# Kernel optimization log

Hardware: AMD Instinct MI355X
Metric: run time of the kernel (lower is better)

The kernel has to match this reference:

```python
import jax, jax.numpy as jnp
import numpy as np

N_GRP = 2048   # n groups
L = 64         # kv slots per group
Q = 4096       # total queries (nq.sum())
D = 256        # d_q = d_k = d_h
DZ = 256       # attention projection dim d_z
DX = 256       # token embedding dim
NTYP = 64      # relation types
NTOK = 50000   # token vocab
M = 131072     # memory tokens
G = 16384      # scatter_sum groups
B = 1024       # examples for scatter_min


def setup_inputs() -> dict:
    key = jax.random.key(0)
    ks = jax.random.split(key, 16)
    q = jax.random.normal(ks[0], (Q, D), jnp.float32)
    k = jax.random.normal(ks[1], (N_GRP, L, D), jnp.float32)
    m = jax.random.bernoulli(ks[2], 0.7, (N_GRP, L))
    m = m.at[:, 0].set(True)  # guarantee >=1 valid slot per group
    # per-query group index == repeat_interleave(arange(n), nq) with nq = 2
    qgrp = jnp.repeat(jnp.arange(N_GRP, dtype=jnp.int32), Q // N_GRP)
    mem = jax.random.randint(ks[3], (M,), 0, NTOK, jnp.int32)
    grp = jnp.sort(jax.random.randint(ks[4], (M,), 0, G, jnp.int32))
    pos2grp = jax.random.randint(ks[5], (N_GRP, L), 0, G, jnp.int32)
    typ = jax.random.randint(ks[6], (Q, NTYP), 0, 2, jnp.int32).astype(bool)
    idx = jnp.sort(jax.random.randint(ks[7], (Q,), 0, B, jnp.int32))
    s = lambda d: 1.0 / np.sqrt(d).astype(np.float32)
    emb = jax.random.normal(ks[8], (NTOK, DX), jnp.float32)
    Wq = jax.random.normal(ks[9], (DZ, D), jnp.float32) * s(D)
    bq = jnp.zeros((DZ,), jnp.float32)
    Wk = jax.random.normal(ks[10], (DZ, D), jnp.float32) * s(D)
    bk = jnp.zeros((DZ,), jnp.float32)
    Wrel = jax.random.normal(ks[11], (NTYP, D + DX), jnp.float32) * s(D + DX)
    brel = jnp.zeros((NTYP,), jnp.float32)
    return dict(q=q, k=k, emb=emb, Wq=Wq, bq=bq, Wk=Wk, bk=bk, Wrel=Wrel,
                brel=brel, m=m, qgrp=qgrp, mem=mem, grp=grp, pos2grp=pos2grp,
                typ=typ, idx=idx)


def reference(q, k, emb, Wq, bq, Wk, bk, Wrel, brel, m, qgrp, mem, grp,
              pos2grp, typ, idx):
    # x_all = scatter_sum(tok_embedding(mem), grp, 0)[pos2grp] : (n, l, dx)
    x_all = jax.ops.segment_sum(emb[mem], grp, num_segments=G)[pos2grp]
    # Attention (ragged masked softmax over l, per-query group gather)
    qz = q @ Wq.T + bq                      # (Q, dz)
    kz = k @ Wk.T + bk                      # (n, l, dz)
    s = jnp.einsum('qd,qld->ql', qz, kz[qgrp]) / np.sqrt(DZ).astype(np.float32)
    s = jnp.where(m[qgrp], s, -jnp.inf)     # masked_fill(~m, -inf)
    p = jax.nn.softmax(s, axis=1)           # softmax over l
    att = jnp.einsum('ql,qld->qd', p, x_all[qgrp])   # (Q, dx)
    logit = jnp.concatenate([q, att], axis=-1) @ Wrel.T + brel  # (Q, n_typ)
    gt = logit > 0
    eq = gt == typ
    acc = eq.astype(jnp.float32).mean()
    em = jax.ops.segment_min(eq.all(1).astype(jnp.int32), idx, num_segments=B)
    emr = em.astype(jnp.float32).mean()
    # binary_cross_entropy_with_logits, reduction='sum', / len(m)
    nll = (jnp.logaddexp(0.0, logit) - logit * typ.astype(logit.dtype)).sum() / N_GRP
    return (logit, acc, emr, nll, em)
```

## Files before the change

### kernel.cpp

```cpp
#include <hip/hip_runtime.h>
#include <hip/hip_bf16.h>
#include <math.h>

#define N_GRP 2048
#define LSLOT 64
#define NQ    4096
#define DIM   256
#define NTYPE 64
#define MMEM  131072
#define GSEG  16384
#define BEX   1024

#define OFF_SEG   0u
#define OFF_QW    4194304u
#define OFF_MT    5242880u
#define OFF_VB    5308416u
#define OFF_WB    5308672u
#define OFF_SB    5308928u
#define OFF_EM    5308936u
#define OFF_CNT   5309960u
#define OFF_NLL   5309964u
#define OFF_FLAG  5309966u

#define OUT_ACC 262144
#define OUT_EMR 262145
#define OUT_NLL 262146
#define OUT_EM  262147

__device__ __forceinline__ bool rd_bool(const void* p, int i, int mode) {
  if (mode == 0) return ((const int*)p)[i] != 0;
  if (mode == 1) return ((const unsigned char*)p)[i] != 0;
  return ((const float*)p)[i] != 0.f;
}

__global__ __launch_bounds__(256)
void k_pre(const float* __restrict__ Wq, const float* __restrict__ bq,
           const float* __restrict__ Wk, const float* __restrict__ bk,
           const void* __restrict__ typ, float* __restrict__ ws) {
  int b = blockIdx.x, t = threadIdx.x;
  if (b < 256) {
    int j = b;
    float acc = 0.f;
    #pragma unroll 8
    for (int z = 0; z < 256; ++z)
      acc += Wk[z * 256 + t] * Wq[z * 256 + j];
    ws[OFF_MT + (unsigned)j * 256 + t] = acc;
  } else if (b == 256) {
    float a = 0.f;
    #pragma unroll 8
    for (int z = 0; z < 256; ++z) a += Wq[z * 256 + t] * bk[z];
    ws[OFF_VB + t] = a;
  } else if (b == 257) {
    float a = 0.f;
    #pragma unroll 8
    for (int z = 0; z < 256; ++z) a += Wk[z * 256 + t] * bq[z];
    ws[OFF_WB + t] = a;
    __shared__ float red[256];
    red[t] = bq[t] * bk[t];
    __syncthreads();
    for (int st = 128; st; st >>= 1) { if (t < st) red[t] += red[t + st]; __syncthreads(); }
    if (t == 0) ws[OFF_SB] = red[0];
  } else {
    __shared__ int fl_f, fl_b;
    if (t == 0) { fl_f = 0; fl_b = 0; }
    __syncthreads();
    for (int i = t; i < 4096; i += 256) {
      unsigned wv = ((const unsigned*)typ)[i];
      if (wv == 0x3F800000u) atomicOr(&fl_f, 1);
      else if (wv > 1u)      atomicOr(&fl_b, 1);
    }
    __syncthreads();
    int* em = (int*)(ws + OFF_EM);
    for (int i = t; i < BEX; i += 256) em[i] = 0x7FFFFFFF;
    if (t == 0) {
      *(int*)(ws + OFF_FLAG) = fl_f ? 2 : (fl_b ? 1 : 0);
      *(int*)(ws + OFF_CNT) = 0;
      *(double*)(ws + OFF_NLL) = 0.0;
    }
  }
}

__global__ __launch_bounds__(256)
void k_segqw(const float* __restrict__ emb, const int* __restrict__ mem,
             const int* __restrict__ grp, const float* __restrict__ q,
             float* __restrict__ ws) {
  int t = threadIdx.x;
  if (blockIdx.x < GSEG / 4) {
    int lane = t & 63, w = t >> 6;
    int g = blockIdx.x * 4 + w;
    int lo = 0, hi = MMEM;
    while (lo < hi) { int mid = (lo + hi) >> 1; if (grp[mid] < g) lo = mid + 1; else hi = mid; }
    int lo2 = lo, hi2 = MMEM;
    while (lo2 < hi2) { int mid = (lo2 + hi2) >> 1; if (grp[mid] < g + 1) lo2 = mid + 1; else hi2 = mid; }
    int n = lo2 - lo;
    int nv = n < 64 ? n : 64;
    int tok = (lane < nv) ? mem[lo + lane] : 0;
    float4 acc = {0.f, 0.f, 0.f, 0.f};
    int r = 0;
    for (; r + 4 <= nv; r += 4) {
      int t0 = __shfl(tok, r + 0), t1 = __shfl(tok, r + 1);
      int t2 = __shfl(tok, r + 2), t3 = __shfl(tok, r + 3);
      float4 v0 = *(const float4*)(emb + (size_t)t0 * 256 + lane * 4);
      float4 v1 = *(const float4*)(emb + (size_t)t1 * 256 + lane * 4);
      float4 v2 = *(const float4*)(emb + (size_t)t2 * 256 + lane * 4);
      float4 v3 = *(const float4*)(emb + (size_t)t3 * 256 + lane * 4);
      acc.x += (v0.x + v1.x) + (v2.x + v3.x);
      acc.y += (v0.y + v1.y) + (v2.y + v3.y);
      acc.z += (v0.z + v1.z) + (v2.z + v3.z);
      acc.w += (v0.w + v1.w) + (v2.w + v3.w);
    }
    for (; r < nv; ++r) {
      int tr = __shfl(tok, r);
      float4 v = *(const float4*)(emb + (size_t)tr * 256 + lane * 4);
      acc.x += v.x; acc.y += v.y; acc.z += v.z; acc.w += v.w;
    }
    for (int rr = lo + 64; rr < lo2; ++rr) {
      int tr = mem[rr];
      float4 v = *(const float4*)(emb + (size_t)tr * 256 + lane * 4);
      acc.x += v.x; acc.y += v.y; acc.z += v.z; acc.w += v.w;
    }
    *(float4*)(ws + OFF_SEG + (size_t)g * 256 + lane * 4) = acc;
  } else {
    int b = blockIdx.x - GSEG / 4;
    int r0 = b * 8;
    const float* MT = ws + OFF_MT;
    float acc[8];
    float wbv = ws[OFF_WB + t];
    #pragma unroll
    for (int r = 0; r < 8; ++r) acc[r] = wbv;
    for (int j = 0; j < 256; j += 4) {
      float m0 = MT[(j + 0) * 256 + t];
      float m1 = MT[(j + 1) * 256 + t];
      float m2 = MT[(j + 2) * 256 + t];
      float m3 = MT[(j + 3) * 256 + t];
      #pragma unroll
      for (int r = 0; r < 8; ++r) {
        float4 q4 = *(const float4*)(q + (size_t)(r0 + r) * 256 + j);
        acc[r] += q4.x * m0 + q4.y * m1 + q4.z * m2 + q4.w * m3;
      }
    }
    #pragma unroll
    for (int r = 0; r < 8; ++r) ws[OFF_QW + (unsigned)(r0 + r) * 256 + t] = acc[r];
  }
}

__global__ __launch_bounds__(256)
void k_attn(const float* __restrict__ q, const float* __restrict__ k,
            const float* __restrict__ Wrel, const float* __restrict__ brel,
            const void* __restrict__ mmask, const int* __restrict__ pos2grp,
            const void* __restrict__ typ, const int* __restrict__ idx,
            float* __restrict__ ws, float* __restrict__ out) {
  int g = blockIdx.x;
  int t = threadIdx.x;
  int lane = t & 63, w = t >> 6;
  __shared__ float qw_l[2][256], qr_l[2][256], att_l[2][256];
  __shared__ float s_raw[2][64], p_l[2][64];
  __shared__ float att_p[4][2][64][4];
  __shared__ float cq_l[2];
  __shared__ float nll_l;
  __shared__ int eqcnt_l, all_l[2];
  const int q0 = 2 * g;
  const int mode = *(const int*)(ws + OFF_FLAG);

  qw_l[0][t] = ws[OFF_QW + (unsigned)q0 * 256 + t];
  qw_l[1][t] = ws[OFF_QW + (unsigned)(q0 + 1) * 256 + t];
  qr_l[0][t] = q[(size_t)q0 * 256 + t];
  qr_l[1][t] = q[(size_t)(q0 + 1) * 256 + t];
  if (t == 0) { eqcnt_l = 0; nll_l = 0.f; }
  if (w < 2) {
    const float* qrow = q + (size_t)(q0 + w) * 256;
    float p = 0.f;
    #pragma unroll
    for (int u = 0; u < 4; ++u) p += qrow[lane + 64 * u] * ws[OFF_VB + lane + 64 * u];
    for (int off = 32; off; off >>= 1) p += __shfl_xor(p, off);
    if (lane == 0) cq_l[w] = p + ws[OFF_SB];
  }
  __syncthreads();

  {
    int sl = w * 16 + (lane >> 2);
    int c4 = lane & 3;
    const float* kr = k + (size_t)g * LSLOT * 256 + (size_t)sl * 256 + c4 * 4;
    float s0 = 0.f, s1 = 0.f;
    #pragma unroll
    for (int j = 0; j < 16; ++j) {
      float4 kv = *(const float4*)(kr + j * 16);
      float4 w0 = *(const float4*)&qw_l[0][j * 16 + c4 * 4];
      float4 w1 = *(const float4*)&qw_l[1][j * 16 + c4 * 4];
      s0 += kv.x * w0.x + kv.y * w0.y + kv.z * w0.z + kv.w * w0.w;
      s1 += kv.x * w1.x + kv.y * w1.y + kv.z * w1.z + kv.w * w1.w;
    }
    s0 += __shfl_xor(s0, 1); s0 += __shfl_xor(s0, 2);
    s1 += __shfl_xor(s1, 1); s1 += __shfl_xor(s1, 2);
    if (c4 == 0) { s_raw[0][sl] = s0; s_raw[1][sl] = s1; }
  }
  __syncthreads();

  if (w < 2) {
    bool valid = rd_bool(mmask, g * LSLOT + lane, mode);
    float v = valid ? (s_raw[w][lane] + cq_l[w]) * 0.0625f : -INFINITY;
    float mx = v;
    for (int off = 32; off; off >>= 1) mx = fmaxf(mx, __shfl_xor(mx, off));
    float e = expf(v - mx);
    float ssum = e;
    for (int off = 32; off; off >>= 1) ssum += __shfl_xor(ssum, off);
    p_l[w][lane] = e / ssum;
  }
  __syncthreads();

  {
    float4 a0 = {0.f,0.f,0.f,0.f}, a1 = {0.f,0.f,0.f,0.f};
    const float* seg = ws + OFF_SEG;
    const int* pg = pos2grp + g * LSLOT;
    #pragma unroll 4
    for (int li = 0; li < 16; ++li) {
      int l = li * 4 + w;
      float p0 = p_l[0][l], p1 = p_l[1][l];
      if (p0 == 0.f && p1 == 0.f) continue;
      int row = pg[l];
      float4 v = *(const float4*)(seg + (size_t)row * 256 + lane * 4);
      a0.x += p0 * v.x; a0.y += p0 * v.y; a0.z += p0 * v.z; a0.w += p0 * v.w;
      a1.x += p1 * v.x; a1.y += p1 * v.y; a1.z += p1 * v.z; a1.w += p1 * v.w;
    }
    *(float4*)&att_p[w][0][lane][0] = a0;
    *(float4*)&att_p[w][1][lane][0] = a1;
  }
  __syncthreads();
  {
    int dl = t >> 2, dc = t & 3;
    #pragma unroll
    for (int qi = 0; qi < 2; ++qi)
      att_l[qi][t] = att_p[0][qi][dl][dc] + att_p[1][qi][dl][dc]
                   + att_p[2][qi][dl][dc] + att_p[3][qi][dl][dc];
  }
  __syncthreads();

  {
    int qi = w >> 1;
    int c4 = lane & 3;
    #pragma unroll
    for (int h = 0; h < 2; ++h) {
      int tt = (w & 1) * 32 + h * 16 + (lane >> 2);
      const float* wr = Wrel + (size_t)tt * 512 + c4 * 4;
      float s = 0.f;
      #pragma unroll
      for (int j = 0; j < 16; ++j) {
        float4 wv = *(const float4*)(wr + j * 16);
        float4 xv = *(const float4*)&qr_l[qi][j * 16 + c4 * 4];
        s += wv.x * xv.x + wv.y * xv.y + wv.z * xv.z + wv.w * xv.w;
      }
      #pragma unroll
      for (int j = 0; j < 16; ++j) {
        float4 wv = *(const float4*)(wr + 1024 + j * 16);
        float4 xv = *(const float4*)&att_l[qi][j * 16 + c4 * 4];
        s += wv.x * xv.x + wv.y * xv.y + wv.z * xv.z + wv.w * xv.w;
      }
      s += __shfl_xor(s, 1); s += __shfl_xor(s, 2);
      if (c4 == 0) s_raw[qi][tt] = s;
    }
  }
  __syncthreads();

  if (w < 2) {
    int qi = w;
    float lg = s_raw[qi][lane] + brel[lane];
    out[(size_t)(q0 + qi) * NTYPE + lane] = lg;
    bool gt = lg > 0.f;
    bool tv = rd_bool(typ, (q0 + qi) * NTYPE + lane, mode);
    bool eqv = (gt == tv);
    unsigned long long mask = __ballot(eqv);
    float nllp = fmaxf(lg, 0.f) + log1pf(expf(-fabsf(lg))) - (tv ? lg : 0.f);
    for (int off = 32; off; off >>= 1) nllp += __shfl_xor(nllp, off);
    if (lane == 0) {
      all_l[qi] = (mask == 0xFFFFFFFFFFFFFFFFull) ? 1 : 0;
      atomicAdd(&eqcnt_l, (int)__popcll(mask));
      atomicAdd(&nll_l, nllp);
    }
  }
  __syncthreads();
  if (t == 0) {
    atomicAdd((int*)(ws + OFF_CNT), eqcnt_l);
    atomicAdd((double*)(ws + OFF_NLL), (double)nll_l);
    int* em = (int*)(ws + OFF_EM);
    atomicMin(&em[idx[q0]], all_l[0]);
    atomicMin(&em[idx[q0 + 1]], all_l[1]);
  }
}

__global__ __launch_bounds__(256)
void k_fin(float* __restrict__ ws, float* __restrict__ out) {
  __shared__ float red[256];
  int t = threadIdx.x;
  const int* em = (const int*)(ws + OFF_EM);
  float s = 0.f;
  for (int i = t; i < BEX; i += 256) {
    float v = (float)em[i];
    out[OUT_EM + i] = v;
    s += v;
  }
  red[t] = s; __syncthreads();
  for (int st = 128; st; st >>= 1) { if (t < st) red[t] += red[t + st]; __syncthreads(); }
  if (t == 0) {
    out[OUT_ACC] = (float)(*(const int*)(ws + OFF_CNT)) / (float)(NQ * NTYPE);
    out[OUT_EMR] = red[0] / (float)BEX;
    out[OUT_NLL] = (float)((*(const double*)(ws + OFF_NLL)) / (double)N_GRP);
  }
}

extern "C" void kernel_launch(void* const* d_in, const int* in_sizes, int n_in,
                              void* d_out, int out_size, void* d_ws, size_t ws_size,
                              hipStream_t stream) {
  const float* q    = (const float*)d_in[0];
  const float* k    = (const float*)d_in[1];
  const float* emb  = (const float*)d_in[2];
  const float* Wq   = (const float*)d_in[3];
  const float* bq   = (const float*)d_in[4];
  const float* Wk   = (const float*)d_in[5];
  const float* bk   = (const float*)d_in[6];
  const float* Wrel = (const float*)d_in[7];
  const float* brel = (const float*)d_in[8];
  const void* mmask   = d_in[9];
  const int* mem      = (const int*)d_in[11];
  const int* grp      = (const int*)d_in[12];
  const int* pos2grp  = (const int*)d_in[13];
  const void* typ     = d_in[14];
  const int* idx      = (const int*)d_in[15];
  float* ws  = (float*)d_ws;
  float* out = (float*)d_out;

  k_pre  <<<259,            256, 0, stream>>>(Wq, bq, Wk, bk, typ, ws);
  k_segqw<<<GSEG/4 + NQ/8,  256, 0, stream>>>(emb, mem, grp, q, ws);
  k_attn <<<N_GRP,          256, 0, stream>>>(q, k, Wrel, brel, mmask, pos2grp, typ, idx, ws, out);
  k_fin  <<<1,              256, 0, stream>>>(ws, out);
}
```

Measured before the change: 386.8 us.

## Split attention kernel, precompute segment pointers, skip masked key slots

Replaces the per-group binary searches with a CSR pointer array built in the prep kernel, used when the workspace is large enough. Moves the query-bias dot product into the projection kernel. Splits the fused attention kernel into a scoring kernel, which skips loading key rows for masked slots, and a separate attention-plus-logit kernel. The softmax probabilities are passed between the two through the output buffer. This cuts search and key-load traffic, but adds a kernel launch and a global round trip.

```diff
diff --git a/kernel.cpp b/kernel.cpp
--- a/kernel.cpp
+++ b/kernel.cpp
@@ -21,6 +21,9 @@
 #define OFF_CNT   5309960u
 #define OFF_NLL   5309964u
 #define OFF_FLAG  5309966u
+#define OFF_CQ    5310208u
+#define OFF_PTR   5314304u
+#define WS_NEED_PTR ((size_t)(OFF_PTR + GSEG + 1) * 4)
 
 #define OUT_ACC 262144
 #define OUT_EMR 262145
@@ -36,15 +39,19 @@
 __global__ __launch_bounds__(256)
 void k_pre(const float* __restrict__ Wq, const float* __restrict__ bq,
            const float* __restrict__ Wk, const float* __restrict__ bk,
-           const void* __restrict__ typ, float* __restrict__ ws) {
+           const void* __restrict__ typ, const int* __restrict__ grp,
+           float* __restrict__ ws, int use_ptr) {
   int b = blockIdx.x, t = threadIdx.x;
   if (b < 256) {
     int j = b;
-    float acc = 0.f;
-    #pragma unroll 8
-    for (int z = 0; z < 256; ++z)
-      acc += Wk[z * 256 + t] * Wq[z * 256 + j];
-    ws[OFF_MT + (unsigned)j * 256 + t] = acc;
+    float a0 = 0.f, a1 = 0.f, a2 = 0.f, a3 = 0.f;
+    for (int z = 0; z < 256; z += 4) {
+      a0 += Wk[(z + 0) * 256 + t] * Wq[(z + 0) * 256 + j];
+      a1 += Wk[(z + 1) * 256 + t] * Wq[(z + 1) * 256 + j];
+      a2 += Wk[(z + 2) * 256 + t] * Wq[(z + 2) * 256 + j];
+      a3 += Wk[(z + 3) * 256 + t] * Wq[(z + 3) * 256 + j];
+    }
+    ws[OFF_MT + (unsigned)j * 256 + t] = (a0 + a1) + (a2 + a3);
   } else if (b == 256) {
     float a = 0.f;
     #pragma unroll 8
@@ -60,7 +67,7 @@
     __syncthreads();
     for (int st = 128; st; st >>= 1) { if (t < st) red[t] += red[t + st]; __syncthreads(); }
     if (t == 0) ws[OFF_SB] = red[0];
-  } else {
+  } else if (b == 258) {
     __shared__ int fl_f, fl_b;
     if (t == 0) { fl_f = 0; fl_b = 0; }
     __syncthreads();
@@ -77,21 +84,37 @@
       *(int*)(ws + OFF_CNT) = 0;
       *(double*)(ws + OFF_NLL) = 0.0;
     }
+  } else {
+    if (!use_ptr) return;
+    int i = (b - 259) * 256 + t;
+    int gi = grp[i];
+    int gp = (i == 0) ? -1 : grp[i - 1];
+    int* ptr = (int*)(ws + OFF_PTR);
+    for (int gg = gp + 1; gg <= gi; ++gg) ptr[gg] = i;
+    if (i == MMEM - 1)
+      for (int gg = gi + 1; gg <= GSEG; ++gg) ptr[gg] = MMEM;
   }
 }
 
 __global__ __launch_bounds__(256)
 void k_segqw(const float* __restrict__ emb, const int* __restrict__ mem,
              const int* __restrict__ grp, const float* __restrict__ q,
-             float* __restrict__ ws) {
+             float* __restrict__ ws, int use_ptr) {
   int t = threadIdx.x;
   if (blockIdx.x < GSEG / 4) {
     int lane = t & 63, w = t >> 6;
     int g = blockIdx.x * 4 + w;
-    int lo = 0, hi = MMEM;
-    while (lo < hi) { int mid = (lo + hi) >> 1; if (grp[mid] < g) lo = mid + 1; else hi = mid; }
-    int lo2 = lo, hi2 = MMEM;
-    while (lo2 < hi2) { int mid = (lo2 + hi2) >> 1; if (grp[mid] < g + 1) lo2 = mid + 1; else hi2 = mid; }
+    int lo, lo2;
+    if (use_ptr) {
+      const int* ptr = (const int*)(ws + OFF_PTR);
+      lo = ptr[g]; lo2 = ptr[g + 1];
+    } else {
+      int l0 = 0, h0 = MMEM;
+      while (l0 < h0) { int mid = (l0 + h0) >> 1; if (grp[mid] < g) l0 = mid + 1; else h0 = mid; }
+      lo = l0; int l1 = l0, h1 = MMEM;
+      while (l1 < h1) { int mid = (l1 + h1) >> 1; if (grp[mid] < g + 1) l1 = mid + 1; else h1 = mid; }
+      lo2 = l1;
+    }
     int n = lo2 - lo;
     int nv = n < 64 ? n : 64;
     int tok = (lane < nv) ? mem[lo + lane] : 0;
@@ -124,88 +147,101 @@
     int b = blockIdx.x - GSEG / 4;
     int r0 = b * 8;
     const float* MT = ws + OFF_MT;
-    float acc[8];
+    float acc[8], cq[8];
     float wbv = ws[OFF_WB + t];
     #pragma unroll
-    for (int r = 0; r < 8; ++r) acc[r] = wbv;
+    for (int r = 0; r < 8; ++r) { acc[r] = wbv; cq[r] = 0.f; }
     for (int j = 0; j < 256; j += 4) {
       float m0 = MT[(j + 0) * 256 + t];
       float m1 = MT[(j + 1) * 256 + t];
       float m2 = MT[(j + 2) * 256 + t];
       float m3 = MT[(j + 3) * 256 + t];
+      float4 vb4 = *(const float4*)(ws + OFF_VB + j);
       #pragma unroll
       for (int r = 0; r < 8; ++r) {
         float4 q4 = *(const float4*)(q + (size_t)(r0 + r) * 256 + j);
         acc[r] += q4.x * m0 + q4.y * m1 + q4.z * m2 + q4.w * m3;
+        cq[r] += q4.x * vb4.x + q4.y * vb4.y + q4.z * vb4.z + q4.w * vb4.w;
       }
     }
     #pragma unroll
     for (int r = 0; r < 8; ++r) ws[OFF_QW + (unsigned)(r0 + r) * 256 + t] = acc[r];
-  }
-}
-
-__global__ __launch_bounds__(256)
-void k_attn(const float* __restrict__ q, const float* __restrict__ k,
-            const float* __restrict__ Wrel, const float* __restrict__ brel,
-            const void* __restrict__ mmask, const int* __restrict__ pos2grp,
-            const void* __restrict__ typ, const int* __restrict__ idx,
-            float* __restrict__ ws, float* __restrict__ out) {
-  int g = blockIdx.x;
-  int t = threadIdx.x;
+    if (t == 0) {
+      float sb = ws[OFF_SB];
+      #pragma unroll
+      for (int r = 0; r < 8; ++r) ws[OFF_CQ + r0 + r] = cq[r] + sb;
+    }
+  }
+}
+
+__global__ __launch_bounds__(256)
+void k_score(const float* __restrict__ k, const void* __restrict__ mmask,
+             float* __restrict__ ws, float* __restrict__ out) {
+  int g = blockIdx.x, t = threadIdx.x;
   int lane = t & 63, w = t >> 6;
-  __shared__ float qw_l[2][256], qr_l[2][256], att_l[2][256];
-  __shared__ float s_raw[2][64], p_l[2][64];
-  __shared__ float att_p[4][2][64][4];
-  __shared__ float cq_l[2];
-  __shared__ float nll_l;
-  __shared__ int eqcnt_l, all_l[2];
+  __shared__ float qw_l[2][256];
+  __shared__ float s_raw[2][64];
   const int q0 = 2 * g;
   const int mode = *(const int*)(ws + OFF_FLAG);
 
   qw_l[0][t] = ws[OFF_QW + (unsigned)q0 * 256 + t];
   qw_l[1][t] = ws[OFF_QW + (unsigned)(q0 + 1) * 256 + t];
-  qr_l[0][t] = q[(size_t)q0 * 256 + t];
-  qr_l[1][t] = q[(size_t)(q0 + 1) * 256 + t];
-  if (t == 0) { eqcnt_l = 0; nll_l = 0.f; }
-  if (w < 2) {
-    const float* qrow = q + (size_t)(q0 + w) * 256;
-    float p = 0.f;
-    #pragma unroll
-    for (int u = 0; u < 4; ++u) p += qrow[lane + 64 * u] * ws[OFF_VB + lane + 64 * u];
-    for (int off = 32; off; off >>= 1) p += __shfl_xor(p, off);
-    if (lane == 0) cq_l[w] = p + ws[OFF_SB];
-  }
   __syncthreads();
 
   {
     int sl = w * 16 + (lane >> 2);
     int c4 = lane & 3;
-    const float* kr = k + (size_t)g * LSLOT * 256 + (size_t)sl * 256 + c4 * 4;
-    float s0 = 0.f, s1 = 0.f;
-    #pragma unroll
-    for (int j = 0; j < 16; ++j) {
-      float4 kv = *(const float4*)(kr + j * 16);
-      float4 w0 = *(const float4*)&qw_l[0][j * 16 + c4 * 4];
-      float4 w1 = *(const float4*)&qw_l[1][j * 16 + c4 * 4];
-      s0 += kv.x * w0.x + kv.y * w0.y + kv.z * w0.z + kv.w * w0.w;
-      s1 += kv.x * w1.x + kv.y * w1.y + kv.z * w1.z + kv.w * w1.w;
-    }
-    s0 += __shfl_xor(s0, 1); s0 += __shfl_xor(s0, 2);
-    s1 += __shfl_xor(s1, 1); s1 += __shfl_xor(s1, 2);
-    if (c4 == 0) { s_raw[0][sl] = s0; s_raw[1][sl] = s1; }
+    bool valid = rd_bool(mmask, g * LSLOT + sl, mode);
+    if (valid) {
+      const float* kr = k + (size_t)g * LSLOT * 256 + (size_t)sl * 256 + c4 * 4;
+      float s0 = 0.f, s1 = 0.f;
+      #pragma unroll
+      for (int j = 0; j < 16; ++j) {
+        float4 kv = *(const float4*)(kr + j * 16);
+        float4 w0 = *(const float4*)&qw_l[0][j * 16 + c4 * 4];
+        float4 w1 = *(const float4*)&qw_l[1][j * 16 + c4 * 4];
+        s0 += kv.x * w0.x + kv.y * w0.y + kv.z * w0.z + kv.w * w0.w;
+        s1 += kv.x * w1.x + kv.y * w1.y + kv.z * w1.z + kv.w * w1.w;
+      }
+      s0 += __shfl_xor(s0, 1); s0 += __shfl_xor(s0, 2);
+      s1 += __shfl_xor(s1, 1); s1 += __shfl_xor(s1, 2);
+      if (c4 == 0) { s_raw[0][sl] = s0; s_raw[1][sl] = s1; }
+    }
   }
   __syncthreads();
 
   if (w < 2) {
     bool valid = rd_bool(mmask, g * LSLOT + lane, mode);
-    float v = valid ? (s_raw[w][lane] + cq_l[w]) * 0.0625f : -INFINITY;
+    float cq = ws[OFF_CQ + q0 + w];
+    float v = valid ? (s_raw[w][lane] + cq) * 0.0625f : -INFINITY;
     float mx = v;
     for (int off = 32; off; off >>= 1) mx = fmaxf(mx, __shfl_xor(mx, off));
     float e = expf(v - mx);
     float ssum = e;
     for (int off = 32; off; off >>= 1) ssum += __shfl_xor(ssum, off);
-    p_l[w][lane] = e / ssum;
-  }
+    out[(size_t)(q0 + w) * NTYPE + lane] = e / ssum;
+  }
+}
+
+__global__ __launch_bounds__(256)
+void k_attlogit(const float* __restrict__ q, const float* __restrict__ Wrel,
+                const float* __restrict__ brel, const int* __restrict__ pos2grp,
+                const void* __restrict__ typ, const int* __restrict__ idx,
+                float* __restrict__ ws, float* __restrict__ out) {
+  int g = blockIdx.x, t = threadIdx.x;
+  int lane = t & 63, w = t >> 6;
+  __shared__ float qr_l[2][256], att_l[2][256];
+  __shared__ float p_l[2][64], lg_l[2][64];
+  __shared__ float att_p[4][2][64][4];
+  __shared__ float nll_l;
+  __shared__ int eqcnt_l, all_l[2];
+  const int q0 = 2 * g;
+  const int mode = *(const int*)(ws + OFF_FLAG);
+
+  qr_l[0][t] = q[(size_t)q0 * 256 + t];
+  qr_l[1][t] = q[(size_t)(q0 + 1) * 256 + t];
+  if (w < 2) p_l[w][lane] = out[(size_t)(q0 + w) * NTYPE + lane];
+  if (t == 0) { eqcnt_l = 0; nll_l = 0.f; }
   __syncthreads();
 
   {
@@ -256,14 +292,14 @@
         s += wv.x * xv.x + wv.y * xv.y + wv.z * xv.z + wv.w * xv.w;
       }
       s += __shfl_xor(s, 1); s += __shfl_xor(s, 2);
-      if (c4 == 0) s_raw[qi][tt] = s;
+      if (c4 == 0) lg_l[qi][tt] = s;
     }
   }
   __syncthreads();
 
   if (w < 2) {
     int qi = w;
-    float lg = s_raw[qi][lane] + brel[lane];
+    float lg = lg_l[qi][lane] + brel[lane];
     out[(size_t)(q0 + qi) * NTYPE + lane] = lg;
     bool gt = lg > 0.f;
     bool tv = rd_bool(typ, (q0 + qi) * NTYPE + lane, mode);
@@ -327,9 +363,11 @@
   const int* idx      = (const int*)d_in[15];
   float* ws  = (float*)d_ws;
   float* out = (float*)d_out;
-
-  k_pre  <<<259,            256, 0, stream>>>(Wq, bq, Wk, bk, typ, ws);
-  k_segqw<<<GSEG/4 + NQ/8,  256, 0, stream>>>(emb, mem, grp, q, ws);
-  k_attn <<<N_GRP,          256, 0, stream>>>(q, k, Wrel, brel, mmask, pos2grp, typ, idx, ws, out);
-  k_fin  <<<1,              256, 0, stream>>>(ws, out);
-}
+  int use_ptr = (ws_size >= WS_NEED_PTR) ? 1 : 0;
+
+  k_pre     <<<259 + MMEM/256, 256, 0, stream>>>(Wq, bq, Wk, bk, typ, grp, ws, use_ptr);
+  k_segqw   <<<GSEG/4 + NQ/8,  256, 0, stream>>>(emb, mem, grp, q, ws, use_ptr);
+  k_score   <<<N_GRP,          256, 0, stream>>>(k, mmask, ws, out);
+  k_attlogit<<<N_GRP,          256, 0, stream>>>(q, Wrel, brel, pos2grp, typ, idx, ws, out);
+  k_fin     <<<1,              256, 0, stream>>>(ws, out);
+}
```

Result: slower. 404.3 us (+4.5%).
